# Optimization experiments

Measured on AMD Instinct MI355X. Metric: run time of the kernel, lower is better.

## Reference

```python
import jax, jax.numpy as jnp
import numpy as np

B, LQ, C = 2, 21760, 256
NH, NL, NP = 8, 4, 4
HD = C // NH  # 32
SPATIAL = np.array([[128, 128], [64, 64], [32, 32], [16, 16]], dtype=np.int64)
START = np.array([0, 16384, 20480, 21504], dtype=np.int64)


def setup_inputs() -> dict:
    key = jax.random.key(0)
    ks = jax.random.split(key, 12)
    inp = {
        "query": jax.random.normal(ks[0], (B, LQ, C), jnp.float32),
        "reference_points": jax.random.uniform(ks[1], (B, LQ, NL, 2), jnp.float32),
        "input_flatten": jax.random.normal(ks[2], (B, LQ, C), jnp.float32),
        "input_spatial_shapes": jnp.asarray(SPATIAL),
        "input_level_start_index": jnp.asarray(START),
        # learned params (random small init so offsets stay reasonable)
        "W_off": jax.random.normal(ks[3], (C, NH * NL * NP * 2), jnp.float32) * 0.01,
        "b_off": jax.random.normal(ks[4], (NH * NL * NP * 2,), jnp.float32) * 0.5,
        "W_attn": jax.random.normal(ks[5], (C, NH * NL * NP), jnp.float32) * 0.02,
        "b_attn": jnp.zeros((NH * NL * NP,), jnp.float32),
        "W_val": jax.random.normal(ks[6], (C, C), jnp.float32) * (1.0 / np.sqrt(C)),
        "b_val": jnp.zeros((C,), jnp.float32),
        "W_out": jax.random.normal(ks[7], (C, C), jnp.float32) * (1.0 / np.sqrt(C)),
        "b_out": jnp.zeros((C,), jnp.float32),
    }
    return inp


def _bilinear_sample(v, loc, H, W):
    """v: (BH, H*W, D); loc: (BH, Q, P, 2) in [0,1] (x, y).
    F.grid_sample bilinear, padding_mode='zeros', align_corners=False.
    Returns (BH, Q, P, D)."""
    BH, Q, P, _ = loc.shape
    x = loc[..., 0] * W - 0.5
    y = loc[..., 1] * H - 0.5
    x0 = jnp.floor(x)
    y0 = jnp.floor(y)
    wx1 = x - x0
    wy1 = y - y0

    def corner(xi, yi, w):
        valid = (xi >= 0) & (xi < W) & (yi >= 0) & (yi < H)
        xi_c = jnp.clip(xi, 0, W - 1).astype(jnp.int32)
        yi_c = jnp.clip(yi, 0, H - 1).astype(jnp.int32)
        idx = (yi_c * W + xi_c).reshape(BH, Q * P)
        g = jnp.take_along_axis(v, idx[..., None], axis=1).reshape(BH, Q, P, -1)
        return g * (w * valid)[..., None]

    out = corner(x0, y0, (1.0 - wx1) * (1.0 - wy1))
    out = out + corner(x0 + 1.0, y0, wx1 * (1.0 - wy1))
    out = out + corner(x0, y0 + 1.0, (1.0 - wx1) * wy1)
    out = out + corner(x0 + 1.0, y0 + 1.0, wx1 * wy1)
    return out


def ms_deform_attn(query, reference_points, input_flatten, shapes_np,
                   W_off, b_off, W_attn, b_attn, W_val, b_val, W_out, b_out):
    Bq, Lq, _ = query.shape
    Len_in = input_flatten.shape[1]
    # value projection -> (B*NH, Len_in, HD)
    value = input_flatten @ W_val + b_val
    value = value.reshape(Bq, Len_in, NH, HD).transpose(0, 2, 1, 3).reshape(Bq * NH, Len_in, HD)
    # sampling offsets / attention weights
    offsets = (query @ W_off + b_off).reshape(Bq, Lq, NH, NL, NP, 2)
    attn = jax.nn.softmax((query @ W_attn + b_attn).reshape(Bq, Lq, NH, NL * NP), axis=-1)
    attn = attn.reshape(Bq, Lq, NH, NL, NP)
    # normalizer is (W_l, H_l) per level, matching (x, y) coordinate order
    normalizer = jnp.stack([jnp.asarray(shapes_np[:, 1], jnp.float32),
                            jnp.asarray(shapes_np[:, 0], jnp.float32)], axis=-1)  # (NL, 2)
    loc = reference_points[:, :, None, :, None, :] + offsets / normalizer[None, None, None, :, None, :]
    # (B, Lq, NH, NL, NP, 2) -> (B, NH, Lq, NL, NP, 2) -> (B*NH, Lq, NL, NP, 2)
    loc = loc.transpose(0, 2, 1, 3, 4, 5).reshape(Bq * NH, Lq, NL, NP, 2)
    attn_bh = attn.transpose(0, 2, 1, 3, 4).reshape(Bq * NH, Lq, NL, NP)

    out = jnp.zeros((Bq * NH, Lq, HD), value.dtype)
    start = 0
    for lvl in range(NL):
        Hc, Wc = int(shapes_np[lvl, 0]), int(shapes_np[lvl, 1])
        v_l = value[:, start:start + Hc * Wc]            # (BH, H*W, D)
        samp = _bilinear_sample(v_l, loc[:, :, lvl], Hc, Wc)  # (BH, Lq, P, D)
        out = out + jnp.einsum('bqpd,bqp->bqd', samp, attn_bh[:, :, lvl])
        start += Hc * Wc
    out = out.reshape(Bq, NH, Lq, HD).transpose(0, 2, 1, 3).reshape(Bq, Lq, C)
    return out @ W_out + b_out


def reference(query, reference_points, input_flatten, input_spatial_shapes,
              input_level_start_index, W_off, b_off, W_attn, b_attn,
              W_val, b_val, W_out, b_out):
    shapes_np = np.asarray(input_spatial_shapes)  # static level shapes
    return ms_deform_attn(query, reference_points, input_flatten, shapes_np,
                          W_off, b_off, W_attn, b_attn, W_val, b_val, W_out, b_out)
```

## Files before the change

### kernel.cpp

```cpp
#include <hip/hip_runtime.h>
#include <hip/hip_fp16.h>
#include <type_traits>

#define LQ 21760
#define MROWS 43520
#define LEN 21760

typedef __attribute__((ext_vector_type(8))) _Float16 half8;
typedef __attribute__((ext_vector_type(4))) float f32x4;

__device__ __forceinline__ uint pkh(float a, float b) {
  auto v = __builtin_amdgcn_cvt_pkrtz(a, b);
  return __builtin_bit_cast(uint, v);
}
__device__ __forceinline__ ushort h16(float x) {
  return __half_as_ushort(__float2half(x));
}
__device__ __forceinline__ float hlo(uint u) {
  return __half2float(__ushort_as_half((ushort)(u & 0xffffu)));
}
__device__ __forceinline__ float hhi(uint u) {
  return __half2float(__ushort_as_half((ushort)(u >> 16)));
}

__device__ __forceinline__ int swz8(int row, int k8) {
  return row * 32 + ((k8 ^ (row & 3) ^ ((row >> 2) & 3)) << 3);
}

template <int BN, bool SPLIT, bool VT, typename AT, typename OT>
__device__ __forceinline__ void gemm_body(
    const AT* __restrict__ A, int lda, const ushort* __restrict__ WT,
    const float* __restrict__ bias, const float* __restrict__ bias2,
    OT* __restrict__ Cout, int ldc, ushort* __restrict__ C2, int mblk,
    ushort* Asb, ushort* Bsb) {
  constexpr int WN = BN / 4;
  constexpr int NI = WN / 16;
  constexpr int BSTEP = (BN * 4) / 512;
  const int tid = threadIdx.x;
  const int m0 = mblk * 128;
  const int w = tid >> 6, wm = w >> 2, wn = w & 3;
  const int l = tid & 63, lr = l & 15, lk = l >> 4;
  const int arow = tid >> 2, ak8 = tid & 3;

  f32x4 acc[4][NI];
#pragma unroll
  for (int mi = 0; mi < 4; ++mi)
#pragma unroll
    for (int ni = 0; ni < NI; ++ni) acc[mi][ni] = {0.f, 0.f, 0.f, 0.f};

  float4 aF0, aF1;
  uint4 aR;
  uint4 bR[BSTEP];

  auto loadA = [&](int k0) {
    const AT* src = A + (size_t)(m0 + arow) * lda + k0 + ak8 * 8;
    if constexpr (std::is_same_v<AT, float>) {
      aF0 = *(const float4*)src;
      aF1 = *(const float4*)(src + 4);
    } else {
      aR = *(const uint4*)src;
    }
  };
  auto loadB = [&](int k0) {
#pragma unroll
    for (int i = 0; i < BSTEP; ++i) {
      int s = tid + i * 512;
      bR[i] = *(const uint4*)(WT + (size_t)(s >> 2) * 256 + k0 + (s & 3) * 8);
    }
  };
  auto writeLDS = [&](int cur) {
    ushort* Ab = Asb + cur * (128 * 32);
    ushort* Bb = Bsb + cur * (BN * 32);
    uint4 pk;
    if constexpr (std::is_same_v<AT, float>)
      pk = make_uint4(pkh(aF0.x, aF0.y), pkh(aF0.z, aF0.w),
                      pkh(aF1.x, aF1.y), pkh(aF1.z, aF1.w));
    else
      pk = aR;
    *(uint4*)&Ab[swz8(arow, ak8)] = pk;
#pragma unroll
    for (int i = 0; i < BSTEP; ++i) {
      int s = tid + i * 512;
      *(uint4*)&Bb[swz8(s >> 2, s & 3)] = bR[i];
    }
  };

  loadA(0);
  loadB(0);
#pragma unroll
  for (int ks = 0; ks < 8; ++ks) {
    const int cur = ks & 1;
    writeLDS(cur);
    __syncthreads();
    if (ks < 7) {
      loadA((ks + 1) * 32);
      loadB((ks + 1) * 32);
    }
    const ushort* Ab = Asb + cur * (128 * 32);
    const ushort* Bb = Bsb + cur * (BN * 32);
    half8 af[4], bfr[NI];
#pragma unroll
    for (int mi = 0; mi < 4; ++mi)
      af[mi] = *(const half8*)&Ab[swz8(wm * 64 + mi * 16 + lr, lk)];
#pragma unroll
    for (int ni = 0; ni < NI; ++ni)
      bfr[ni] = *(const half8*)&Bb[swz8(wn * WN + ni * 16 + lr, lk)];
#pragma unroll
    for (int mi = 0; mi < 4; ++mi)
#pragma unroll
      for (int ni = 0; ni < NI; ++ni)
        acc[mi][ni] = __builtin_amdgcn_mfma_f32_16x16x32_f16(
            af[mi], bfr[ni], acc[mi][ni], 0, 0, 0);
  }
#pragma unroll
  for (int mi = 0; mi < 4; ++mi) {
#pragma unroll
    for (int ni = 0; ni < NI; ++ni) {
      int col = wn * WN + ni * 16 + lr;
      float bs;
      if constexpr (SPLIT)
        bs = (col < 256) ? bias[col] : bias2[col - 256];
      else
        bs = bias[col];
      int row = m0 + wm * 64 + mi * 16 + lk * 4;
#pragma unroll
      for (int r = 0; r < 4; ++r) {
        float v = acc[mi][ni][r] + bs;
        if constexpr (SPLIT) {
          if (col < 256)
            ((ushort*)Cout)[(size_t)(row + r) * 256 + col] = h16(v);
          else
            C2[(size_t)(row + r) * 128 + col - 256] = h16(v);
        } else if constexpr (VT) {
          int rr = row + r;
          int bb = (rr >= LQ) ? 1 : 0;
          int pos = rr - bb * LQ;
          size_t idx =
              ((size_t)(bb * 8 + (col >> 5)) * LQ + pos) * 32 + (col & 31);
          ((ushort*)Cout)[idx] = h16(v);
        } else if constexpr (std::is_same_v<OT, ushort>) {
          Cout[(size_t)(row + r) * ldc + col] = h16(v);
        } else {
          Cout[(size_t)(row + r) * ldc + col] = v;
        }
      }
    }
  }
}

__global__ __launch_bounds__(512) void gemm_front(
    const float* __restrict__ inpf, const ushort* __restrict__ WTv,
    const float* __restrict__ bval, ushort* __restrict__ value16,
    const float* __restrict__ query, const ushort* __restrict__ WTol,
    const float* __restrict__ boff, const float* __restrict__ battn,
    ushort* __restrict__ off16, ushort* __restrict__ logit16) {
  __shared__ ushort Asb[2 * 128 * 32];
  __shared__ ushort Bsb[2 * 384 * 32];
  int bid = blockIdx.x;
  if (bid < 340) {
    gemm_body<256, false, true, float, ushort>(
        inpf, 256, WTv, bval, nullptr, value16, 256, nullptr, bid, Asb, Bsb);
  } else {
    gemm_body<384, true, false, float, ushort>(query, 256, WTol, boff, battn,
                                               off16, 256, logit16, bid - 340,
                                               Asb, Bsb);
  }
}

__global__ __launch_bounds__(512) void gemm_out(
    const ushort* __restrict__ midb, const ushort* __restrict__ WTu,
    const float* __restrict__ bout, float* __restrict__ outp) {
  __shared__ ushort Asb[2 * 128 * 32];
  __shared__ ushort Bsb[2 * 256 * 32];
  gemm_body<256, false, false, ushort, float>(midb, 512, WTu, bout, nullptr,
                                              outp, 256, nullptr, blockIdx.x,
                                              Asb, Bsb);
}

__global__ __launch_bounds__(256) void wt_cvt_all(
    const float* __restrict__ Wval, const float* __restrict__ Woff,
    const float* __restrict__ Wattn, const float* __restrict__ Wout,
    ushort* __restrict__ WTv, ushort* __restrict__ WTol,
    ushort* __restrict__ WTu) {
  int i = blockIdx.x * 256 + threadIdx.x;
  if (i < 65536) {
    int n = i >> 8, k = i & 255;
    WTv[i] = h16(Wval[(size_t)k * 256 + n]);
  } else if (i < 163840) {
    int j = i - 65536;
    int n = j >> 8, k = j & 255;
    float s = (n < 256) ? Woff[(size_t)k * 256 + n] : Wattn[(size_t)k * 128 + n - 256];
    WTol[j] = h16(s);
  } else {
    int j = i - 163840;
    int n = j >> 8, k = j & 255;
    WTu[j] = h16(Wout[(size_t)k * 256 + n]);
  }
}

__global__ __launch_bounds__(256) void msda_sample(
    const ushort* __restrict__ off16,
    const ushort* __restrict__ logit16,
    const float* __restrict__ refpts,
    const ushort* __restrict__ value,
    ushort* __restrict__ midb) {
  __shared__ float prs[64][16];
  __shared__ float refs[32][4][2];
  __shared__ int tix[1024][4];
  __shared__ uint twp[1024][2];

  const int bid = blockIdx.x;
  const int grp = bid & 7;
  const int sub = bid >> 3;
  const int b = grp >> 2;
  const int hp = grp & 3;
  const int q0 = sub * 32;
  const int tid = threadIdx.x;
  const size_t fqB = (size_t)b * LQ + q0;

  {
    int q = tid >> 3, r = tid & 7;
    refs[q][r >> 1][r & 1] = refpts[(fqB + q) * 8 + r];
  }
  if (tid < 64) {
    int q = tid >> 1, hh = tid & 1;
    int h = hp * 2 + hh;
    const uint4* lp = (const uint4*)(logit16 + (fqB + q) * 128 + h * 16);
    uint4 p0 = lp[0], p1 = lp[1];
    float v[16] = {hlo(p0.x), hhi(p0.x), hlo(p0.y), hhi(p0.y),
                   hlo(p0.z), hhi(p0.z), hlo(p0.w), hhi(p0.w),
                   hlo(p1.x), hhi(p1.x), hlo(p1.y), hhi(p1.y),
                   hlo(p1.z), hhi(p1.z), hlo(p1.w), hhi(p1.w)};
    float m = v[0];
#pragma unroll
    for (int i = 1; i < 16; ++i) m = fmaxf(m, v[i]);
    float s = 0.f;
#pragma unroll
    for (int i = 0; i < 16; ++i) { v[i] = __expf(v[i] - m); s += v[i]; }
    float inv = 1.0f / s;
#pragma unroll
    for (int i = 0; i < 16; ++i) prs[tid][i] = v[i] * inv;
  }
  __syncthreads();

#pragma unroll
  for (int i = 0; i < 4; ++i) {
    int t = tid + i * 256;
    int q = t >> 5;
    int hh = (t >> 4) & 1;
    int lp_ = t & 15;
    int lvl = lp_ >> 2;
    int h = hp * 2 + hh;
    uint op = ((const uint*)off16)[(fqB + q) * 128 + h * 16 + lp_];
    float ox = hlo(op), oy = hhi(op);
    float aw = prs[q * 2 + hh][lp_];
    float rx = refs[q][lvl][0], ry = refs[q][lvl][1];
    int Wl = 128 >> lvl;
    int st = (lvl == 0) ? 0 : ((lvl == 1) ? 16384 : ((lvl == 2) ? 20480 : 21504));
    float fW = (float)Wl;
    float invW = 1.0f / fW;
    float x = (rx + ox * invW) * fW - 0.5f;
    float y = (ry + oy * invW) * fW - 0.5f;
    float x0f = floorf(x), y0f = floorf(y);
    float wx1 = x - x0f, wy1 = y - y0f;
    float wx0 = 1.f - wx1, wy0 = 1.f - wy1;
    int x0 = (int)x0f, y0 = (int)y0f;
    int x1 = x0 + 1, y1 = y0 + 1;
    bool vx0 = (x0 >= 0) & (x0 < Wl), vx1 = (x1 >= 0) & (x1 < Wl);
    bool vy0 = (y0 >= 0) & (y0 < Wl), vy1 = (y1 >= 0) & (y1 < Wl);
    int xc0 = min(max(x0, 0), Wl - 1);
    int yc0 = min(max(y0, 0), Wl - 1), yc1 = min(max(y1, 0), Wl - 1);
    float w00 = (vx0 && vy0) ? wx0 * wy0 * aw : 0.f;
    float w10 = (vx1 && vy0) ? wx1 * wy0 * aw : 0.f;
    float w01 = (vx0 && vy1) ? wx0 * wy1 * aw : 0.f;
    float w11 = (vx1 && vy1) ? wx1 * wy1 * aw : 0.f;
    bool xs = (x0 < 0);
    float lo0 = xs ? w10 : w00, hi0 = xs ? 0.f : w10;
    float lo1 = xs ? w11 : w01, hi1 = xs ? 0.f : w11;
    int baseB = (h * LQ + st + yc0 * Wl + xc0) * 64;
    int dyB = (yc1 - yc0) * Wl * 64;
    int slot = (t & ~15) | ((lp_ + (t >> 5)) & 15);
    tix[slot][0] = baseB;
    tix[slot][1] = dyB;
    twp[slot][0] = pkh(lo0, hi0);
    twp[slot][1] = pkh(lo1, hi1);
  }
  __syncthreads();

  const int g8 = tid >> 3;
  const int dl = tid & 7;
  const uint dlB = (uint)dl * 16u;
  const uint sh = (uint)((tid & 4) << 2);
  const char* vb0c = (const char*)(value + (size_t)b * (LEN * 256));

#define PKC(ACC, U, WP)                                                 \
  asm("v_pk_fma_f16 %0, %1, %2, %0 op_sel:[0,0,0] op_sel_hi:[1,0,1]"    \
      : "+v"(ACC)                                                       \
      : "v"(U), "v"(WP))
#define PROMO1(ALO, AHI, C)                                             \
  asm("v_fma_mix_f32 %0, 1.0, %1, %0 op_sel:[0,0,0] op_sel_hi:[0,1,0]"  \
      : "+v"(ALO) : "v"(C));                                            \
  asm("v_fma_mix_f32 %0, 1.0, %1, %0 op_sel:[0,1,0] op_sel_hi:[0,1,0]"  \
      : "+v"(AHI) : "v"(C));                                            \
  C = 0u;

#pragma unroll
  for (int half = 0; half < 2; ++half) {
    const int qh = g8 * 2 + half;
    const int tb2 = qh * 16;
    float a0 = 0.f, a1 = 0.f, a2 = 0.f, a3 = 0.f;
    float a4 = 0.f, a5 = 0.f, a6 = 0.f, a7 = 0.f;
    uint c0 = 0u, c1 = 0u, c2 = 0u, c3 = 0u;
#pragma unroll 4
    for (int t = 0; t < 16; ++t) {
      int slot = tb2 + ((t + g8) & 15);
      int2 bx = *(const int2*)&tix[slot][0];
      uint2 wp = *(const uint2*)&twp[slot][0];
      const char* p0 = vb0c + (uint)bx.x + dlB;
      uint4 u0 = *(const uint4*)p0;
      uint4 u1 = *(const uint4*)(p0 + (uint)bx.y);
      uint wp0 = wp.x >> sh;
      uint wp1 = wp.y >> sh;
      PKC(c0, u0.x, wp0); PKC(c1, u0.y, wp0);
      PKC(c2, u0.z, wp0); PKC(c3, u0.w, wp0);
      PKC(c0, u1.x, wp1); PKC(c1, u1.y, wp1);
      PKC(c2, u1.z, wp1); PKC(c3, u1.w, wp1);
      if ((t & 3) == 3) {
        PROMO1(a0, a1, c0);
        PROMO1(a2, a3, c1);
        PROMO1(a4, a5, c2);
        PROMO1(a6, a7, c3);
      }
    }
    a0 += __shfl_xor(a0, 4); a1 += __shfl_xor(a1, 4);
    a2 += __shfl_xor(a2, 4); a3 += __shfl_xor(a3, 4);
    a4 += __shfl_xor(a4, 4); a5 += __shfl_xor(a5, 4);
    a6 += __shfl_xor(a6, 4); a7 += __shfl_xor(a7, 4);
    if (dl < 4) {
      const int q = qh >> 1, h = hp * 2 + (qh & 1);
      ushort* mp = midb + (fqB + q) * 512 + h * 32 + dl * 8;
      *(uint4*)mp =
          make_uint4(pkh(a0, a1), pkh(a2, a3), pkh(a4, a5), pkh(a6, a7));
    }
  }
#undef PROMO1
#undef PKC
}

extern "C" void kernel_launch(void* const* d_in, const int* in_sizes, int n_in,
                              void* d_out, int out_size, void* d_ws,
                              size_t ws_size, hipStream_t stream) {
  (void)in_sizes; (void)n_in; (void)out_size; (void)ws_size;
  const float* query = (const float*)d_in[0];
  const float* refp  = (const float*)d_in[1];
  const float* inpf  = (const float*)d_in[2];
  const float* Woff  = (const float*)d_in[5];
  const float* boff  = (const float*)d_in[6];
  const float* Wattn = (const float*)d_in[7];
  const float* battn = (const float*)d_in[8];
  const float* Wval  = (const float*)d_in[9];
  const float* bval  = (const float*)d_in[10];
  const float* Wout  = (const float*)d_in[11];
  const float* bout  = (const float*)d_in[12];

  ushort* value16 = (ushort*)d_ws;
  ushort* off16   = value16 + (size_t)MROWS * 256;
  ushort* logit16 = off16 + (size_t)MROWS * 256;
  ushort* WTv     = logit16 + (size_t)MROWS * 128;
  ushort* WTol    = WTv + 65536;
  ushort* WTu     = WTol + 98304;

  ushort* midb = (ushort*)d_out;

  wt_cvt_all<<<896, 256, 0, stream>>>(Wval, Woff, Wattn, Wout, WTv, WTol, WTu);

  gemm_front<<<680, 512, 0, stream>>>(inpf, WTv, bval, value16, query, WTol,
                                      boff, battn, off16, logit16);

  msda_sample<<<MROWS / 8, 256, 0, stream>>>(off16, logit16, refp, value16,
                                             midb);

  gemm_out<<<MROWS / 128, 512, 0, stream>>>(midb, WTu, bout, (float*)d_out);
}
```

Measured before the change: 128.0 us.

## Load GEMM tiles directly into LDS with global_load_lds and swizzled sources

Replaces the register-staged global-to-LDS copies of the weight tile, and of the A tile when A is fp16, with direct global_load_lds transfers. Because the hardware writes LDS lane-contiguously, the XOR swizzle moves onto the global source address instead of the LDS address. This cuts VGPR staging and LDS store instructions in the GEMM main loop. It depends on the barrier waiting for the outstanding direct loads before the next tile is read, and fp32 A inputs still go through registers.

```diff
diff --git a/kernel.cpp b/kernel.cpp
--- a/kernel.cpp
+++ b/kernel.cpp
@@ -25,6 +25,12 @@
 
 __device__ __forceinline__ int swz8(int row, int k8) {
   return row * 32 + ((k8 ^ (row & 3) ^ ((row >> 2) & 3)) << 3);
+}
+
+__device__ __forceinline__ void gll16(const void* g, void* l) {
+  __builtin_amdgcn_global_load_lds(
+      (const __attribute__((address_space(1))) unsigned int*)g,
+      (__attribute__((address_space(3))) unsigned int*)l, 16, 0, 0);
 }
 
 template <int BN, bool SPLIT, bool VT, typename AT, typename OT>
@@ -36,6 +42,7 @@
   constexpr int WN = BN / 4;
   constexpr int NI = WN / 16;
   constexpr int BSTEP = (BN * 4) / 512;
+  constexpr bool GLA = std::is_same_v<AT, ushort>;
   const int tid = threadIdx.x;
   const int m0 = mblk * 128;
   const int w = tid >> 6, wm = w >> 2, wn = w & 3;
@@ -49,52 +56,51 @@
     for (int ni = 0; ni < NI; ++ni) acc[mi][ni] = {0.f, 0.f, 0.f, 0.f};
 
   float4 aF0, aF1;
-  uint4 aR;
-  uint4 bR[BSTEP];
 
   auto loadA = [&](int k0) {
     const AT* src = A + (size_t)(m0 + arow) * lda + k0 + ak8 * 8;
     if constexpr (std::is_same_v<AT, float>) {
       aF0 = *(const float4*)src;
       aF1 = *(const float4*)(src + 4);
-    } else {
-      aR = *(const uint4*)src;
     }
   };
-  auto loadB = [&](int k0) {
+  auto writeA = [&](int cur) {
+    ushort* Ab = Asb + cur * (128 * 32);
+    uint4 pk = make_uint4(pkh(aF0.x, aF0.y), pkh(aF0.z, aF0.w),
+                          pkh(aF1.x, aF1.y), pkh(aF1.z, aF1.w));
+    *(uint4*)&Ab[swz8(arow, ak8)] = pk;
+  };
+  auto gllB = [&](int k0, int cur) {
+    ushort* Bb = Bsb + cur * (BN * 32);
 #pragma unroll
     for (int i = 0; i < BSTEP; ++i) {
       int s = tid + i * 512;
-      bR[i] = *(const uint4*)(WT + (size_t)(s >> 2) * 256 + k0 + (s & 3) * 8);
+      int row = s >> 2;
+      int k8e = (s & 3) ^ (row & 3) ^ ((row >> 2) & 3);
+      gll16(WT + (size_t)row * 256 + k0 + k8e * 8,
+            Bb + (size_t)(i * 512 + (tid & ~63)) * 8);
     }
   };
-  auto writeLDS = [&](int cur) {
+  auto gllA = [&](int k0, int cur) {
     ushort* Ab = Asb + cur * (128 * 32);
-    ushort* Bb = Bsb + cur * (BN * 32);
-    uint4 pk;
-    if constexpr (std::is_same_v<AT, float>)
-      pk = make_uint4(pkh(aF0.x, aF0.y), pkh(aF0.z, aF0.w),
-                      pkh(aF1.x, aF1.y), pkh(aF1.z, aF1.w));
-    else
-      pk = aR;
-    *(uint4*)&Ab[swz8(arow, ak8)] = pk;
-#pragma unroll
-    for (int i = 0; i < BSTEP; ++i) {
-      int s = tid + i * 512;
-      *(uint4*)&Bb[swz8(s >> 2, s & 3)] = bR[i];
-    }
+    int row = tid >> 2;
+    int k8e = (tid & 3) ^ (row & 3) ^ ((row >> 2) & 3);
+    gll16((const ushort*)A + (size_t)(m0 + row) * lda + k0 + k8e * 8,
+          Ab + (size_t)(tid & ~63) * 8);
   };
 
-  loadA(0);
-  loadB(0);
+  if constexpr (!GLA) loadA(0);
+  if constexpr (GLA) gllA(0, 0);
+  gllB(0, 0);
 #pragma unroll
   for (int ks = 0; ks < 8; ++ks) {
     const int cur = ks & 1;
-    writeLDS(cur);
+    if constexpr (!GLA) writeA(cur);
     __syncthreads();
     if (ks < 7) {
-      loadA((ks + 1) * 32);
-      loadB((ks + 1) * 32);
+      if constexpr (GLA) gllA((ks + 1) * 32, cur ^ 1);
+      gllB((ks + 1) * 32, cur ^ 1);
+      if constexpr (!GLA) loadA((ks + 1) * 32);
     }
     const ushort* Ab = Asb + cur * (128 * 32);
     const ushort* Bb = Bsb + cur * (BN * 32);
```

Result: faster. 123.1 us (-3.8%).
